# Kernel tuning notes

Hardware: AMD Instinct MI355X
Metric: run time of the kernel (lower is better)

Reference implementation:

```python
import jax, jax.numpy as jnp
import numpy as np

BLOCKSIZE = 64  # bitsandbytes default quantization block size

# NF4 codebook (bitsandbytes normal-float 4-bit quantiles)
NF4_CODE = jnp.array([
    -1.0, -0.6961928009986877, -0.5250730514526367, -0.39491748809814453,
    -0.28444138169288635, -0.18477343022823334, -0.09105003625154495, 0.0,
    0.07958029955625534, 0.16093020141124725, 0.24611230194568634,
    0.33791524171829224, 0.44070982933044434, 0.5626170039176941,
    0.7229568362236023, 1.0], dtype=jnp.float32)

IN_FEATURES = 4096
OUT_FEATURES = 16384
TOKENS = 8192  # batch 4 * seq 2048, flattened


def setup_inputs() -> dict:
    key = jax.random.key(0)
    k1, k2, k3, k4 = jax.random.split(key, 4)
    x = jax.random.normal(k1, (TOKENS, IN_FEATURES), dtype=jnp.float32)
    codes = jax.random.randint(k2, (OUT_FEATURES, IN_FEATURES), 0, 16, dtype=jnp.int32)
    n_blocks = OUT_FEATURES * IN_FEATURES // BLOCKSIZE
    absmax = jax.random.uniform(k3, (n_blocks,), dtype=jnp.float32)
    bias = jax.random.normal(k4, (OUT_FEATURES,), dtype=jnp.float32)
    return {"x": x, "codes": codes, "absmax": absmax, "bias": bias}


def _dequant_nf4(codes, absmax):
    # codes: [O, I] int in [0,16); absmax: [O*I/BLOCKSIZE] per-block scale
    O, I = codes.shape
    w = NF4_CODE[codes]                        # [O, I] codebook lookup
    w = w.reshape(-1, BLOCKSIZE) * absmax[:, None]  # block-wise rescale
    return w.reshape(O, I)


def reference(x, codes, absmax, bias):
    w = _dequant_nf4(codes, absmax)            # [O, I]
    return jnp.dot(x, w.T) + bias              # [T, O]
```

## Files before the change

### kernel.cpp

```cpp
#include <hip/hip_runtime.h>
#include <hip/hip_bf16.h>
#include <stdint.h>

#define TOKENS 8192
#define IN_F   4096
#define OUT_F  16384

typedef __bf16 bf16;
typedef __bf16 bf16x8 __attribute__((ext_vector_type(8)));
typedef float  f32x4  __attribute__((ext_vector_type(4)));

__device__ __constant__ float NF4[16] = {
    -1.0f, -0.6961928009986877f, -0.5250730514526367f, -0.39491748809814453f,
    -0.28444138169288635f, -0.18477343022823334f, -0.09105003625154495f, 0.0f,
    0.07958029955625534f, 0.16093020141124725f, 0.24611230194568634f,
    0.33791524171829224f, 0.44070982933044434f, 0.5626170039176941f,
    0.7229568362236023f, 1.0f};

__global__ __launch_bounds__(256) void cvt_kernel(const float* __restrict__ x,
                                                  bf16* __restrict__ xb) {
    size_t base = ((size_t)blockIdx.x * blockDim.x + threadIdx.x) * 8;
    float4 a = *(const float4*)(x + base);
    float4 b = *(const float4*)(x + base + 4);
    bf16x8 w;
    w[0] = (bf16)a.x; w[1] = (bf16)a.y; w[2] = (bf16)a.z; w[3] = (bf16)a.w;
    w[4] = (bf16)b.x; w[5] = (bf16)b.y; w[6] = (bf16)b.z; w[7] = (bf16)b.w;
    *(bf16x8*)(xb + base) = w;
}

__global__ __launch_bounds__(256) void dequant_kernel(const int* __restrict__ codes,
                                                      const float* __restrict__ absmax,
                                                      bf16* __restrict__ W) {
    __shared__ float lut[16];
    if (threadIdx.x < 16) lut[threadIdx.x] = NF4[threadIdx.x];
    __syncthreads();
    size_t base = ((size_t)blockIdx.x * blockDim.x + threadIdx.x) * 8;
    float scale = absmax[base >> 6];
    int4 c0 = *(const int4*)(codes + base);
    int4 c1 = *(const int4*)(codes + base + 4);
    bf16x8 w;
    w[0] = (bf16)(lut[c0.x] * scale);
    w[1] = (bf16)(lut[c0.y] * scale);
    w[2] = (bf16)(lut[c0.z] * scale);
    w[3] = (bf16)(lut[c0.w] * scale);
    w[4] = (bf16)(lut[c1.x] * scale);
    w[5] = (bf16)(lut[c1.y] * scale);
    w[6] = (bf16)(lut[c1.z] * scale);
    w[7] = (bf16)(lut[c1.w] * scale);
    *(bf16x8*)(W + base) = w;
}

#define BM 128
#define BN 128
#define BK 32

typedef const unsigned int __attribute__((address_space(1)))* gas_ptr;
typedef unsigned int __attribute__((address_space(3)))* las_ptr;

__device__ __forceinline__ void async_load16(const void* g, void* l) {
    __builtin_amdgcn_global_load_lds((gas_ptr)(uintptr_t)g, (las_ptr)(uintptr_t)l, 16, 0, 0);
}

__global__ __launch_bounds__(256) void gemm_bt(const bf16* __restrict__ A,
                                               const bf16* __restrict__ B,
                                               const float* __restrict__ bias,
                                               float* __restrict__ C) {
    constexpr int M = TOKENS, N = OUT_F, K = IN_F;
    (void)M;
    __shared__ bf16 As[BM * BK];
    __shared__ bf16 Bs[BN * BK];

    const int t = threadIdx.x;
    const int wave = t >> 6, lane = t & 63;
    const int quad = lane >> 4, r16 = lane & 15;
    const int wr = wave >> 1, wc = wave & 1;
    const int m0 = blockIdx.y * BM;
    const int n0 = blockIdx.x * BN;

    f32x4 acc[4][4];
#pragma unroll
    for (int i = 0; i < 4; i++)
#pragma unroll
        for (int j = 0; j < 4; j++) acc[i][j] = (f32x4){0.f, 0.f, 0.f, 0.f};

    const int c0r = t >> 2, c0c = (t & 3) * 8;
    const int c1r = (256 + t) >> 2, c1c = ((256 + t) & 3) * 8;
    bf16* lA0 = As + (size_t)(wave * 64) * 8;
    bf16* lA1 = As + (size_t)(256 + wave * 64) * 8;
    bf16* lB0 = Bs + (size_t)(wave * 64) * 8;
    bf16* lB1 = Bs + (size_t)(256 + wave * 64) * 8;
    const bf16* gA = A + (size_t)m0 * K;
    const bf16* gB = B + (size_t)n0 * K;

    for (int k0 = 0; k0 < K; k0 += BK) {
        async_load16(gA + (size_t)c0r * K + k0 + c0c, lA0);
        async_load16(gA + (size_t)c1r * K + k0 + c1c, lA1);
        async_load16(gB + (size_t)c0r * K + k0 + c0c, lB0);
        async_load16(gB + (size_t)c1r * K + k0 + c1c, lB1);
        __syncthreads();

        bf16x8 af[4], bfr[4];
#pragma unroll
        for (int i = 0; i < 4; i++)
            af[i] = *(const bf16x8*)(As + (wr * 64 + i * 16 + r16) * BK + quad * 8);
#pragma unroll
        for (int j = 0; j < 4; j++)
            bfr[j] = *(const bf16x8*)(Bs + (wc * 64 + j * 16 + r16) * BK + quad * 8);

#pragma unroll
        for (int i = 0; i < 4; i++)
#pragma unroll
            for (int j = 0; j < 4; j++)
                acc[i][j] = __builtin_amdgcn_mfma_f32_16x16x32_bf16(af[i], bfr[j], acc[i][j], 0, 0, 0);
        __syncthreads();
    }

    float bj[4];
#pragma unroll
    for (int j = 0; j < 4; j++) bj[j] = bias[n0 + wc * 64 + j * 16 + r16];
#pragma unroll
    for (int i = 0; i < 4; i++) {
#pragma unroll
        for (int r = 0; r < 4; r++) {
            int m = m0 + wr * 64 + i * 16 + quad * 4 + r;
            float* crow = C + (size_t)m * N + n0 + wc * 64 + r16;
#pragma unroll
            for (int j = 0; j < 4; j++) crow[j * 16] = acc[i][j][r] + bj[j];
        }
    }
}

#define FT 16
__global__ void gemm_fallback(const float* __restrict__ x, const int* __restrict__ codes,
                              const float* __restrict__ absmax, const float* __restrict__ bias,
                              float* __restrict__ C) {
    __shared__ float xs[FT][FT];
    __shared__ float ws_[FT][FT + 1];
    int tx = threadIdx.x, ty = threadIdx.y;
    int n = blockIdx.x * FT + tx;
    int m = blockIdx.y * FT + ty;
    float acc = 0.f;
    for (int k0 = 0; k0 < IN_F; k0 += FT) {
        xs[ty][tx] = x[(size_t)m * IN_F + k0 + tx];
        int o = blockIdx.x * FT + ty;
        size_t widx = (size_t)o * IN_F + k0 + tx;
        ws_[ty][tx] = NF4[codes[widx]] * absmax[widx >> 6];
        __syncthreads();
#pragma unroll
        for (int k = 0; k < FT; k++) acc += xs[ty][k] * ws_[tx][k];
        __syncthreads();
    }
    C[(size_t)m * OUT_F + n] = acc + bias[n];
}

extern "C" void kernel_launch(void* const* d_in, const int* in_sizes, int n_in,
                              void* d_out, int out_size, void* d_ws, size_t ws_size,
                              hipStream_t stream) {
    const float* x      = (const float*)d_in[0];
    const int*   codes  = (const int*)d_in[1];
    const float* absmax = (const float*)d_in[2];
    const float* bias   = (const float*)d_in[3];
    float* out = (float*)d_out;

    const size_t xb_elems = (size_t)TOKENS * IN_F;
    const size_t w_elems  = (size_t)OUT_F * IN_F;
    const size_t need = (xb_elems + w_elems) * sizeof(bf16);

    if (ws_size >= need) {
        bf16* xb = (bf16*)d_ws;
        bf16* W  = xb + xb_elems;
        cvt_kernel<<<(int)(xb_elems / 8 / 256), 256, 0, stream>>>(x, xb);
        dequant_kernel<<<(int)(w_elems / 8 / 256), 256, 0, stream>>>(codes, absmax, W);
        gemm_bt<<<dim3(OUT_F / BN, TOKENS / BM), 256, 0, stream>>>(xb, W, bias, out);
    } else {
        gemm_fallback<<<dim3(OUT_F / FT, TOKENS / FT), dim3(FT, FT), 0, stream>>>(
            x, codes, absmax, bias, out);
    }
}
```

Baseline: 1.927 ms.

## Add 256x256 double-buffered GEMM with swizzled LDS and XCD-aware block mapping

Replaces the 128x128x32 single-buffered bf16 GEMM with a 256x256x64 tile kernel using 512 threads, 128KB of dynamic LDS double-buffered, and an XOR-swizzled layout to avoid bank conflicts. Global-to-LDS async loads for the next tile are issued mid-compute, with partial vmcnt waits so memory traffic overlaps the MFMA clusters. Wave priority is raised around the MFMA clusters, and block indices are remapped across the 8 XCDs to improve L2 locality. It risks lower occupancy from the 128KB LDS footprint, and it falls back to the old kernel if the shared-memory attribute or launch fails.

```diff
diff --git a/kernel.cpp b/kernel.cpp
--- a/kernel.cpp
+++ b/kernel.cpp
@@ -50,16 +50,173 @@
     *(bf16x8*)(W + base) = w;
 }
 
+typedef const unsigned int __attribute__((address_space(1)))* gas_ptr;
+typedef unsigned int __attribute__((address_space(3)))* las_ptr;
+
+__device__ __forceinline__ void async_load16(const void* g, void* l) {
+    __builtin_amdgcn_global_load_lds((gas_ptr)(uintptr_t)g, (las_ptr)(uintptr_t)l, 16, 0, 0);
+}
+
+#define GBM 256
+#define GBN 256
+#define GBK 64
+#define GNT (IN_F / GBK)
+
+__device__ __forceinline__ void bar_nodrain() {
+    __builtin_amdgcn_sched_barrier(0);
+    __builtin_amdgcn_s_barrier();
+    __builtin_amdgcn_sched_barrier(0);
+}
+
+#define CLUSTER(I0, J0)                                                          \
+    do {                                                                         \
+        __builtin_amdgcn_s_setprio(1);                                           \
+        _Pragma("unroll") for (int i_ = 0; i_ < 4; ++i_) {                       \
+            _Pragma("unroll") for (int j_ = 0; j_ < 2; ++j_) {                   \
+                acc[(I0) + i_][(J0) + j_] = __builtin_amdgcn_mfma_f32_16x16x32_bf16( \
+                    a[i_][0], b[(J0) + j_][0], acc[(I0) + i_][(J0) + j_], 0, 0, 0);  \
+                acc[(I0) + i_][(J0) + j_] = __builtin_amdgcn_mfma_f32_16x16x32_bf16( \
+                    a[i_][1], b[(J0) + j_][1], acc[(I0) + i_][(J0) + j_], 0, 0, 0);  \
+            }                                                                    \
+        }                                                                        \
+        __builtin_amdgcn_s_setprio(0);                                           \
+    } while (0)
+
+__global__ __launch_bounds__(512, 2) void gemm256(const bf16* __restrict__ A,
+                                                  const bf16* __restrict__ B,
+                                                  const float* __restrict__ bias,
+                                                  float* __restrict__ C) {
+    constexpr int K = IN_F, N = OUT_F;
+    extern __shared__ char smem[];
+
+    const int t    = threadIdx.x;
+    const int wave = t >> 6, lane = t & 63;
+    const int quad = lane >> 4, r16 = lane & 15;
+    const int wr = wave >> 2, wc = wave & 3;
+
+    const int g  = blockIdx.x;
+    const int s  = (g & 7) * (2048 / 8) + (g >> 3);
+    const int by = s >> 6;
+    const int bx = s & 63;
+    const int m0 = by * GBM;
+    const int n0 = bx * GBN;
+
+    const int wl    = wave * 1024 + lane * 16;
+    const int fwl   = wl ^ (((wl >> 7) & 7) << 4);
+    const int rbase = fwl >> 7;
+    const int cbase = (fwl & 127) >> 1;
+
+    const bf16* pA = A + (size_t)(m0 + rbase) * K + cbase;
+    const bf16* pB = B + (size_t)(n0 + rbase) * K + cbase;
+
+    char* const sA0 = smem;
+    char* const sB0 = smem + 32768;
+    char* const sA1 = smem + 65536;
+    char* const sB1 = smem + 98304;
+    const int wslot = wave * 1024;
+
+#pragma unroll
+    for (int h = 0; h < 2; ++h)
+#pragma unroll
+        for (int i = 0; i < 2; ++i) {
+            const size_t go = (size_t)(h * 128 + i * 64) * K;
+            const int    lo = h * 16384 + i * 8192 + wslot;
+            async_load16(pA + go, sA0 + lo);
+            async_load16(pB + go, sB0 + lo);
+        }
+#pragma unroll
+    for (int h = 0; h < 2; ++h)
+#pragma unroll
+        for (int i = 0; i < 2; ++i) {
+            const size_t go = (size_t)(h * 128 + i * 64) * K;
+            const int    lo = h * 16384 + i * 8192 + wslot;
+            async_load16(pA + GBK + go, sA1 + lo);
+            async_load16(pB + GBK + go, sB1 + lo);
+        }
+    asm volatile("s_waitcnt vmcnt(8)" ::: "memory");
+    bar_nodrain();
+
+    const int sw   = (r16 & 7) << 4;
+    const int c0   = (quad * 16) ^ sw;
+    const int c1   = (64 + quad * 16) ^ sw;
+    const int rowA = (wr * 128 + r16) * 128;
+    const int rowB = (wc * 64 + r16) * 128;
+
+    f32x4 acc[8][4];
+#pragma unroll
+    for (int i = 0; i < 8; ++i)
+#pragma unroll
+        for (int j = 0; j < 4; ++j) acc[i][j] = (f32x4){0.f, 0.f, 0.f, 0.f};
+
+    const bf16* qA = pA + 2 * GBK;
+    const bf16* qB = pB + 2 * GBK;
+
+    for (int kt = 0; kt < GNT; ++kt) {
+        char* const sA = (kt & 1) ? sA1 : sA0;
+        char* const sB = (kt & 1) ? sB1 : sB0;
+        const char* rA = sA + rowA;
+        const char* rB = sB + rowB;
+
+        bf16x8 a[4][2], b[4][2];
+#pragma unroll
+        for (int i = 0; i < 4; ++i) {
+            a[i][0] = *(const bf16x8*)(rA + i * 2048 + c0);
+            a[i][1] = *(const bf16x8*)(rA + i * 2048 + c1);
+        }
+#pragma unroll
+        for (int j = 0; j < 4; ++j) {
+            b[j][0] = *(const bf16x8*)(rB + j * 2048 + c0);
+            b[j][1] = *(const bf16x8*)(rB + j * 2048 + c1);
+        }
+        CLUSTER(0, 0);
+        CLUSTER(0, 2);
+#pragma unroll
+        for (int i = 0; i < 4; ++i) {
+            a[i][0] = *(const bf16x8*)(rA + (i + 4) * 2048 + c0);
+            a[i][1] = *(const bf16x8*)(rA + (i + 4) * 2048 + c1);
+        }
+        CLUSTER(4, 0);
+        bar_nodrain();
+        if (kt < GNT - 2) {
+#pragma unroll
+            for (int h = 0; h < 2; ++h)
+#pragma unroll
+                for (int i = 0; i < 2; ++i) {
+                    const size_t go = (size_t)(h * 128 + i * 64) * K;
+                    const int    lo = h * 16384 + i * 8192 + wslot;
+                    async_load16(qA + go, sA + lo);
+                    async_load16(qB + go, sB + lo);
+                }
+            qA += GBK; qB += GBK;
+        }
+        CLUSTER(4, 2);
+        if (kt < GNT - 2) {
+            asm volatile("s_waitcnt vmcnt(8)" ::: "memory");
+            bar_nodrain();
+        } else if (kt == GNT - 2) {
+            asm volatile("s_waitcnt vmcnt(0)" ::: "memory");
+            bar_nodrain();
+        }
+    }
+
+    float bj[4];
+#pragma unroll
+    for (int j = 0; j < 4; ++j) bj[j] = bias[n0 + wc * 64 + j * 16 + r16];
+#pragma unroll
+    for (int i = 0; i < 8; ++i) {
+#pragma unroll
+        for (int r = 0; r < 4; ++r) {
+            const int m = m0 + wr * 128 + i * 16 + quad * 4 + r;
+            float* crow = C + (size_t)m * N + n0 + wc * 64 + r16;
+#pragma unroll
+            for (int j = 0; j < 4; ++j) crow[j * 16] = acc[i][j][r] + bj[j];
+        }
+    }
+}
+
 #define BM 128
 #define BN 128
 #define BK 32
-
-typedef const unsigned int __attribute__((address_space(1)))* gas_ptr;
-typedef unsigned int __attribute__((address_space(3)))* las_ptr;
-
-__device__ __forceinline__ void async_load16(const void* g, void* l) {
-    __builtin_amdgcn_global_load_lds((gas_ptr)(uintptr_t)g, (las_ptr)(uintptr_t)l, 16, 0, 0);
-}
 
 __global__ __launch_bounds__(256) void gemm_bt(const bf16* __restrict__ A,
                                                const bf16* __restrict__ B,
@@ -171,7 +328,23 @@
         bf16* W  = xb + xb_elems;
         cvt_kernel<<<(int)(xb_elems / 8 / 256), 256, 0, stream>>>(x, xb);
         dequant_kernel<<<(int)(w_elems / 8 / 256), 256, 0, stream>>>(codes, absmax, W);
-        gemm_bt<<<dim3(OUT_F / BN, TOKENS / BM), 256, 0, stream>>>(xb, W, bias, out);
+
+        static int smem_ok = -1;
+        if (smem_ok < 0) {
+            hipError_t e = hipFuncSetAttribute(
+                reinterpret_cast<const void*>(gemm256),
+                hipFuncAttributeMaxDynamicSharedMemorySize, 131072);
+            smem_ok = (e == hipSuccess) ? 1 : 0;
+        }
+        bool launched = false;
+        if (smem_ok) {
+            (void)hipGetLastError();
+            gemm256<<<dim3(2048), 512, 131072, stream>>>(xb, W, bias, out);
+            launched = (hipGetLastError() == hipSuccess);
+        }
+        if (!launched) {
+            gemm_bt<<<dim3(OUT_F / BN, TOKENS / BM), 256, 0, stream>>>(xb, W, bias, out);
+        }
     } else {
         gemm_fallback<<<dim3(OUT_F / FT, TOKENS / FT), dim3(FT, FT), 0, stream>>>(
             x, codes, absmax, bias, out);
```

Result: faster. 1.714 ms (-11.1%).
